# Performance work log

Measured on AMD Instinct MI355X. Metric: run time of the kernel, lower is better.

The kernel has to match this reference:

```python
import jax, jax.numpy as jnp
import numpy as np


def setup_inputs() -> dict:
    key = jax.random.key(0)
    ks = jax.random.split(key, 7)
    B, T, inp_d, hid_d = 16, 4095, 2048, 2048
    scale = 0.02
    return {
        "x": jax.random.normal(ks[0], (B, inp_d), dtype=jnp.float32),
        "K_his": jax.random.normal(ks[1], (B, T, hid_d), dtype=jnp.float32),
        "V_his": jax.random.normal(ks[2], (B, T, hid_d), dtype=jnp.float32),
        "W_attn": jax.random.normal(ks[3], (inp_d, 3 * hid_d), dtype=jnp.float32) * scale,
        "b_attn": jax.random.normal(ks[4], (3 * hid_d,), dtype=jnp.float32) * scale,
        "W_proj": jax.random.normal(ks[5], (hid_d, hid_d), dtype=jnp.float32) * scale,
        "b_proj": jax.random.normal(ks[6], (hid_d,), dtype=jnp.float32) * scale,
        "n_head": 16,
    }


def reference(x, K_his, V_his, W_attn, b_attn, W_proj, b_proj, n_head):
    B = x.shape[0]
    qkv = x @ W_attn + b_attn                      # [B, 3*hid_d]
    q, k, v = jnp.split(qkv, 3, axis=-1)           # each [B, hid_d]
    hid_d = q.shape[-1]
    dh = hid_d // n_head
    # append current step to the KV cache
    K = jnp.concatenate([K_his, k[:, None, :]], axis=1)  # [B, T, hid_d]
    V = jnp.concatenate([V_his, v[:, None, :]], axis=1)
    T = K.shape[1]
    Kh = K.reshape(B, T, n_head, dh).transpose(0, 2, 1, 3)  # [B, H, T, dh]
    Vh = V.reshape(B, T, n_head, dh).transpose(0, 2, 1, 3)  # [B, H, T, dh]
    qh = q.reshape(B, n_head, dh, 1)                        # [B, H, dh, 1]
    scores = Kh @ qh                                        # [B, H, T, 1]
    # NOTE: faithful to the source: softmax over dim=-1 which has size 1 -> all ones
    att = jax.nn.softmax(scores, axis=-1)                   # [B, H, T, 1]
    v_next = jnp.swapaxes(Vh, -1, -2) @ att                 # [B, H, dh, 1]
    v_next = v_next.reshape(B, hid_d) @ W_proj + b_proj     # [B, hid_d]
    # faithful: reshape the head-major layout back to [B, T, hid_d]
    K_out = Kh.reshape(B, -1, hid_d)
    V_out = Vh.reshape(B, -1, hid_d)
    return K_out, V_out, v_next
```

## Files before the change

kernel.cpp:

```cpp
#include <hip/hip_runtime.h>


typedef float f4 __attribute__((ext_vector_type(4)));

__global__ void init_kernel(const float* __restrict__ b_attn,
                            const float* __restrict__ b_proj,
                            float* __restrict__ qkv,
                            float* __restrict__ colsum,
                            float* __restrict__ vnext) {
  int tid = blockIdx.x * blockDim.x + threadIdx.x;
  qkv[tid] = b_attn[2048 + (tid & 4095)];
  if (tid < 32768) {
    colsum[tid] = 0.0f;
    vnext[tid] = b_proj[tid & 2047];
  }
}

__global__ void small_gemm_atomic(const float* __restrict__ X,
                                  const float* __restrict__ W,
                                  int ldw, int col0,
                                  float* __restrict__ out, int ncols) {
  int j  = blockIdx.x * 512 + threadIdx.x * 2;
  int k0 = blockIdx.y * 64;
  const float* wp = W + (size_t)k0 * ldw + col0 + j;
  float2 acc[16];
#pragma unroll
  for (int b = 0; b < 16; ++b) acc[b] = make_float2(0.f, 0.f);
  for (int kk = 0; kk < 64; ++kk) {
    float2 w = *(const float2*)(wp + (size_t)kk * ldw);
    const float* xp = X + k0 + kk;
#pragma unroll
    for (int b = 0; b < 16; ++b) {
      float xv = xp[(size_t)b * 2048];
      acc[b].x = fmaf(xv, w.x, acc[b].x);
      acc[b].y = fmaf(xv, w.y, acc[b].y);
    }
  }
#pragma unroll
  for (int b = 0; b < 16; ++b) {
    atomicAdd(&out[b * ncols + j],     acc[b].x);
    atomicAdd(&out[b * ncols + j + 1], acc[b].y);
  }
}

__global__ void __launch_bounds__(256)
copy_transpose(const float* __restrict__ K_his,
               const float* __restrict__ V_his,
               const float* __restrict__ qkv,
               float* __restrict__ out,
               float* __restrict__ colsum) {
  const int b     = blockIdx.y;
  const int which = blockIdx.z;
  const int i0    = blockIdx.x * 8;
  const int h     = i0 >> 8;
  const int tid   = threadIdx.x;
  const int d     = (tid * 4) & 127;
  const int s0    = tid >> 5;
  const int tb0   = (i0 & 255) * 16;

  const float* src  = which ? V_his : K_his;
  const float* qrow = qkv + b * 4096 + which * 2048 + h * 128 + d;
  const float* base = src + (size_t)b * 8386560ull + (unsigned)(h * 128 + d);
  float* orow = out + ((size_t)which << 27) + ((size_t)b << 23)
                    + (size_t)i0 * 2048u + (unsigned)(tid * 4);

  __shared__ f4 red[128];

  f4 acc = {0.f, 0.f, 0.f, 0.f};
#pragma unroll
  for (int r = 0; r < 8; ++r) {
    const int trow = tb0 + r * 16;
    const int t0 = trow + s0;
    const int t1 = trow + s0 + 8;
    const float* p0 = (t0 == 4095) ? qrow : base + (size_t)t0 * 2048u;
    const float* p1 = (t1 == 4095) ? qrow : base + (size_t)t1 * 2048u;
    f4 v0 = __builtin_nontemporal_load((const f4*)p0);
    f4 v1 = __builtin_nontemporal_load((const f4*)p1);
    __builtin_nontemporal_store(v0, (f4*)(orow + r * 2048));
    __builtin_nontemporal_store(v1, (f4*)(orow + r * 2048 + 1024));
    acc += v0 + v1;
  }

  if (which) {
    acc.x += __shfl_xor(acc.x, 32);
    acc.y += __shfl_xor(acc.y, 32);
    acc.z += __shfl_xor(acc.z, 32);
    acc.w += __shfl_xor(acc.w, 32);
    int lane = tid & 63;
    int wave = tid >> 6;
    if (lane < 32) red[wave * 32 + lane] = acc;
    __syncthreads();
    if (tid < 32) {
      f4 a = red[tid] + red[32 + tid] + red[64 + tid] + red[96 + tid];
      float* cp = colsum + b * 2048 + h * 128 + tid * 4;
      atomicAdd(cp + 0, a.x);
      atomicAdd(cp + 1, a.y);
      atomicAdd(cp + 2, a.z);
      atomicAdd(cp + 3, a.w);
    }
  }
}

extern "C" void kernel_launch(void* const* d_in, const int* in_sizes, int n_in,
                              void* d_out, int out_size, void* d_ws, size_t ws_size,
                              hipStream_t stream) {
  const float* x      = (const float*)d_in[0];
  const float* K_his  = (const float*)d_in[1];
  const float* V_his  = (const float*)d_in[2];
  const float* W_attn = (const float*)d_in[3];
  const float* b_attn = (const float*)d_in[4];
  const float* W_proj = (const float*)d_in[5];
  const float* b_proj = (const float*)d_in[6];

  float* out    = (float*)d_out;
  float* qkv    = (float*)d_ws;
  float* colsum = qkv + 16 * 4096;
  float* vnext  = out + 268435456ull;

  init_kernel<<<256, 256, 0, stream>>>(b_attn, b_proj, qkv, colsum, vnext);
  small_gemm_atomic<<<dim3(8, 32), 256, 0, stream>>>(x, W_attn, 6144, 2048, qkv, 4096);
  copy_transpose<<<dim3(512, 16, 2), 256, 0, stream>>>(K_his, V_his, qkv, out, colsum);
  small_gemm_atomic<<<dim3(4, 32), 256, 0, stream>>>(colsum, W_proj, 2048, 0, vnext, 2048);
}
```

Baseline: 465.5 us.

## Restructure KV copy-transpose to read full rows and swap halves via lane shuffles

The copy_transpose kernel is reorganised so each wave reads contiguous 1 KB row segments (two time steps per iteration) and exchanges half-waves with __shfl_xor. This forms the head-major output rows, replacing the old mapping where each block gathered 512-byte pieces across 16 time rows. Each block now handles four groups, so the grid shrinks to a quarter of the blocks. The LDS reduction and __syncthreads for the V column sum are dropped in favour of per-lane atomics, which means more atomics in total. The aim is better read coalescing and less block-launch overhead in a bandwidth-bound copy, at the cost of extra shuffle instructions and atomic traffic.

```diff
diff --git a/kernel.cpp b/kernel.cpp
--- a/kernel.cpp
+++ b/kernel.cpp
@@ -43,7 +43,7 @@
   }
 }
 
-__global__ void __launch_bounds__(256)
+__global__ void __launch_bounds__(256, 4)
 copy_transpose(const float* __restrict__ K_his,
                const float* __restrict__ V_his,
                const float* __restrict__ qkv,
@@ -51,53 +51,56 @@
                float* __restrict__ colsum) {
   const int b     = blockIdx.y;
   const int which = blockIdx.z;
-  const int i0    = blockIdx.x * 8;
-  const int h     = i0 >> 8;
+  const int x     = blockIdx.x;
   const int tid   = threadIdx.x;
-  const int d     = (tid * 4) & 127;
-  const int s0    = tid >> 5;
-  const int tb0   = (i0 & 255) * 16;
+  const int l     = tid & 63;
+  const int w     = tid >> 6;
+  const int i     = (x & 1) * 4 + w;
+  const int gblk  = x >> 1;
+  const bool hi   = (l >= 32);
 
   const float* src  = which ? V_his : K_his;
-  const float* qrow = qkv + b * 4096 + which * 2048 + h * 128 + d;
-  const float* base = src + (size_t)b * 8386560ull + (unsigned)(h * 128 + d);
-  float* orow = out + ((size_t)which << 27) + ((size_t)b << 23)
-                    + (size_t)i0 * 2048u + (unsigned)(tid * 4);
-
-  __shared__ f4 red[128];
+  const float* srcb = src + (size_t)b * 8386560ull + (unsigned)(i * 256 + 4 * l);
+  const float* qsrc = qkv + b * 4096 + which * 2048 + i * 256 + 4 * l;
+  float* outb = out + ((size_t)which << 27) + ((size_t)b << 23);
 
   f4 acc = {0.f, 0.f, 0.f, 0.f};
+
+  for (int gs = 0; gs < 4; ++gs) {
+    const int g = gblk * 4 + gs;
+    float* row0 = outb + (size_t)(2 * i * 256 + g) * 2048u + (unsigned)(4 * l);
+    float* row1 = row0 + 256 * 2048;
 #pragma unroll
-  for (int r = 0; r < 8; ++r) {
-    const int trow = tb0 + r * 16;
-    const int t0 = trow + s0;
-    const int t1 = trow + s0 + 8;
-    const float* p0 = (t0 == 4095) ? qrow : base + (size_t)t0 * 2048u;
-    const float* p1 = (t1 == 4095) ? qrow : base + (size_t)t1 * 2048u;
-    f4 v0 = __builtin_nontemporal_load((const f4*)p0);
-    f4 v1 = __builtin_nontemporal_load((const f4*)p1);
-    __builtin_nontemporal_store(v0, (f4*)(orow + r * 2048));
-    __builtin_nontemporal_store(v1, (f4*)(orow + r * 2048 + 1024));
-    acc += v0 + v1;
+    for (int rp = 0; rp < 8; ++rp) {
+      const int t0 = g * 16 + rp * 2;
+      const float* r0 = srcb + (size_t)t0 * 2048u;
+      const float* r1 = (t0 + 1 == 4095) ? qsrc : (r0 + 2048);
+      f4 A = __builtin_nontemporal_load((const f4*)r0);
+      f4 B = __builtin_nontemporal_load((const f4*)r1);
+      if (which) acc += A + B;
+      f4 Ax, Bx;
+#pragma unroll
+      for (int c = 0; c < 4; ++c) {
+        Ax[c] = __shfl_xor(A[c], 32);
+        Bx[c] = __shfl_xor(B[c], 32);
+      }
+      f4 H0, H1;
+#pragma unroll
+      for (int c = 0; c < 4; ++c) {
+        H0[c] = hi ? Bx[c] : A[c];
+        H1[c] = hi ? B[c] : Ax[c];
+      }
+      __builtin_nontemporal_store(H0, (f4*)(row0 + rp * 256));
+      __builtin_nontemporal_store(H1, (f4*)(row1 + rp * 256));
+    }
   }
 
   if (which) {
-    acc.x += __shfl_xor(acc.x, 32);
-    acc.y += __shfl_xor(acc.y, 32);
-    acc.z += __shfl_xor(acc.z, 32);
-    acc.w += __shfl_xor(acc.w, 32);
-    int lane = tid & 63;
-    int wave = tid >> 6;
-    if (lane < 32) red[wave * 32 + lane] = acc;
-    __syncthreads();
-    if (tid < 32) {
-      f4 a = red[tid] + red[32 + tid] + red[64 + tid] + red[96 + tid];
-      float* cp = colsum + b * 2048 + h * 128 + tid * 4;
-      atomicAdd(cp + 0, a.x);
-      atomicAdd(cp + 1, a.y);
-      atomicAdd(cp + 2, a.z);
-      atomicAdd(cp + 3, a.w);
-    }
+    float* cp = colsum + b * 2048 + i * 256 + 4 * l;
+    atomicAdd(cp + 0, acc.x);
+    atomicAdd(cp + 1, acc.y);
+    atomicAdd(cp + 2, acc.z);
+    atomicAdd(cp + 3, acc.w);
   }
 }
 
@@ -119,6 +122,6 @@
 
   init_kernel<<<256, 256, 0, stream>>>(b_attn, b_proj, qkv, colsum, vnext);
   small_gemm_atomic<<<dim3(8, 32), 256, 0, stream>>>(x, W_attn, 6144, 2048, qkv, 4096);
-  copy_transpose<<<dim3(512, 16, 2), 256, 0, stream>>>(K_his, V_his, qkv, out, colsum);
+  copy_transpose<<<dim3(128, 16, 2), 256, 0, stream>>>(K_his, V_his, qkv, out, colsum);
   small_gemm_atomic<<<dim3(4, 32), 256, 0, stream>>>(colsum, W_proj, 2048, 0, vnext, 2048);
 }
```

Measured after the change: 456.4 us, median of 2. Within noise of the previous version (-2.0%).
